# Kernel tuning notes

Measured on AMD Instinct MI355X. Metric: run time of the kernel, lower is better.

## Reference

```python
import jax, jax.numpy as jnp
import numpy as np

NUM_EXPERTS = 256
TOP_K = 8
HIDDEN = 7168
N_GROUP = 8
TOPK_GROUP = 4
ROUTED_SCALING_FACTOR = 2.5
NORM_TOPK_PROB = True
TOKENS = 8192


def setup_inputs() -> dict:
    key = jax.random.key(0)
    k1, k2, k3 = jax.random.split(key, 3)
    hidden_states = jax.random.normal(k1, (TOKENS, HIDDEN), dtype=jnp.float32)
    # small init scale keeps router logits in a reasonable sigmoid range
    weight = jax.random.normal(k2, (NUM_EXPERTS, HIDDEN), dtype=jnp.float32) * 0.02
    e_score_correction_bias = jax.random.normal(k3, (NUM_EXPERTS,), dtype=jnp.float32) * 0.01
    return {
        "hidden_states": hidden_states,
        "weight": weight,
        "e_score_correction_bias": e_score_correction_bias,
    }


def reference(hidden_states, weight, e_score_correction_bias):
    hs = hidden_states.reshape(-1, hidden_states.shape[-1]).astype(jnp.float32)
    # [T, E] router logits -> sigmoid scores
    router_logits = hs @ weight.astype(jnp.float32).T
    scores = jax.nn.sigmoid(router_logits)
    scores_for_choice = scores + e_score_correction_bias[None, :]

    experts_per_group = NUM_EXPERTS // N_GROUP
    T = scores_for_choice.shape[0]
    # group score = sum of top-2 biased scores within each group  [T, G]
    grouped = scores_for_choice.reshape(T, N_GROUP, experts_per_group)
    top2_vals, _ = jax.lax.top_k(grouped, 2)
    group_scores = top2_vals.sum(axis=-1)

    # select top groups and build group mask  [T, G]
    _, group_idx = jax.lax.top_k(group_scores, TOPK_GROUP)
    group_mask = jnp.zeros_like(group_scores).at[
        jnp.arange(T)[:, None], group_idx
    ].set(1.0)

    # expand group mask to experts and zero out non-selected groups  [T, E]
    score_mask = jnp.broadcast_to(
        group_mask[:, :, None], (T, N_GROUP, experts_per_group)
    ).reshape(T, NUM_EXPERTS)
    masked_scores = jnp.where(score_mask.astype(bool), scores_for_choice, 0.0)

    # top-k experts over masked biased scores, weights gathered from raw scores
    _, topk_indices = jax.lax.top_k(masked_scores, TOP_K)
    topk_weights = jnp.take_along_axis(scores, topk_indices, axis=1)
    if NORM_TOPK_PROB:
        topk_weights = topk_weights / (
            topk_weights.sum(axis=-1, keepdims=True) + 1e-20
        )
    topk_weights = topk_weights * ROUTED_SCALING_FACTOR
    return topk_indices, topk_weights
```

## Files before the change

### kernel.cpp

```cpp
#include <hip/hip_runtime.h>
#include <float.h>
#include <math.h>

#define TOKENS 8192
#define EXPERTS 256
#define HIDDEN 7168
#define TOPK 8
#define TOPKG 4

#define BM 128
#define BN 256
#define BK 32
#define KSPLIT 4
#define KQ (HIDDEN / KSPLIT)
#define NKTB (KQ / BK)

#define TAU_E 6.0e-6f
#define TAU_G 1.2e-5f
#define MAXFB 1024

#define WIMG_ELEMS 1835008

typedef __attribute__((ext_vector_type(8))) short bf16x8;
typedef __attribute__((ext_vector_type(16))) float f32x16;

__device__ inline ushort bf16_rne(float x) {
    uint u = __float_as_uint(x);
    return (ushort)((u + 0x7FFFu + ((u >> 16) & 1u)) >> 16);
}
__device__ inline float bf16_tof(ushort h) { return __uint_as_float((uint)h << 16); }

#define CVTPK(lo, hi) ({ uint r_; asm("v_cvt_pk_bf16_f32 %0, %1, %2" : "=v"(r_) : "v"(lo), "v"(hi)); r_; })
__device__ inline float lo16f(uint u) { return __uint_as_float(u << 16); }
__device__ inline float hi16f(uint u) { return __uint_as_float(u & 0xFFFF0000u); }

#define BAR() do {                                             \
    asm volatile("s_waitcnt lgkmcnt(0)" ::: "memory");         \
    __builtin_amdgcn_s_barrier();                              \
    __builtin_amdgcn_sched_barrier(0);                         \
} while (0)

__global__ __launch_bounds__(256) void split_w(const float* __restrict__ W,
                                               ushort* __restrict__ wh,
                                               ushort* __restrict__ wl,
                                               int* __restrict__ cnt) {
    if (blockIdx.x == 0 && threadIdx.x == 0) *cnt = 0;
    const int tau  = blockIdx.x * 256 + threadIdx.x;
    const int j    = tau & 7;
    const int lane = (tau >> 3) & 63;
    const int cg   = (tau >> 9) & 7;
    const int kt16 = tau >> 12;
    const int col  = cg * 32 + (lane & 31);
    const int k    = kt16 * 16 + (lane >> 5) * 8 + j;
    const float w  = W[(size_t)col * HIDDEN + k];
    const ushort h = bf16_rne(w);
    const ushort l = bf16_rne(w - bf16_tof(h));
    wh[tau] = h;
    wl[tau] = l;
}

template <bool ATOMIC>
__global__ __launch_bounds__(512, 2) void logits_mfma(const float* __restrict__ A,
                                                      const ushort* __restrict__ wh,
                                                      const ushort* __restrict__ wl,
                                                      float* __restrict__ dst) {
    __shared__ ushort Ah[2][BM * BK];
    __shared__ ushort Al[2][BM * BK];

    const int b  = blockIdx.x;
    const int ks = b & 3;
    const int mb = b >> 2;
    const int row0 = mb * BM;

    const int t = threadIdx.x, lane = t & 63, wid = t >> 6;
    const int wm = wid >> 2, wn = wid & 3;

    const int sr = t >> 2, q = t & 3;
    const float* Ap = A + (size_t)(row0 + sr) * HIDDEN + (size_t)ks * KQ + q * 8;
    const int sswz = ((sr >> 1) ^ (sr >> 3)) & 3;
    const int sidx = sr * 32 + ((q ^ sswz) << 3);

    int fidx[2][2];
    #pragma unroll
    for (int mi = 0; mi < 2; ++mi) {
        const int r = wm * 64 + mi * 32 + (lane & 31);
        const int swz = ((r >> 1) ^ (r >> 3)) & 3;
        #pragma unroll
        for (int kh = 0; kh < 2; ++kh)
            fidx[mi][kh] = r * 32 + (((kh * 2 + (lane >> 5)) ^ swz) << 3);
    }

    const int wlanes = lane * 8;

    f32x16 acc[2][2];
    #pragma unroll
    for (int mi = 0; mi < 2; ++mi)
        #pragma unroll
        for (int n = 0; n < 2; ++n) acc[mi][n] = (f32x16)0.f;

    float4 aA0, aA1, aB0, aB1;
    bf16x8 wAh[2][2], wAl[2][2], wBh[2][2], wBl[2][2];

    #define WLOAD(DH, DL, KTL) do {                                            \
        const size_t wo = ((size_t)((ks * NKTB + (KTL)) * 16 + wn * 2)) * 512 + wlanes; \
        DH[0][0] = *(const bf16x8*)(wh + wo);                                  \
        DH[1][0] = *(const bf16x8*)(wh + wo + 512);                            \
        DH[0][1] = *(const bf16x8*)(wh + wo + 4096);                           \
        DH[1][1] = *(const bf16x8*)(wh + wo + 4608);                           \
        DL[0][0] = *(const bf16x8*)(wl + wo);                                  \
        DL[1][0] = *(const bf16x8*)(wl + wo + 512);                            \
        DL[0][1] = *(const bf16x8*)(wl + wo + 4096);                           \
        DL[1][1] = *(const bf16x8*)(wl + wo + 4608);                           \
    } while (0)

    #define STAGE(BB, R0, R1) do {                                             \
        uint h0 = CVTPK(R0.x, R0.y), h1 = CVTPK(R0.z, R0.w);                   \
        uint h2 = CVTPK(R1.x, R1.y), h3 = CVTPK(R1.z, R1.w);                   \
        float q0 = R0.x - lo16f(h0), q1 = R0.y - hi16f(h0);                    \
        float q2 = R0.z - lo16f(h1), q3 = R0.w - hi16f(h1);                    \
        float q4 = R1.x - lo16f(h2), q5 = R1.y - hi16f(h2);                    \
        float q6 = R1.z - lo16f(h3), q7 = R1.w - hi16f(h3);                    \
        uint l0 = CVTPK(q0, q1), l1 = CVTPK(q2, q3);                           \
        uint l2 = CVTPK(q4, q5), l3 = CVTPK(q6, q7);                           \
        *(uint4*)&Ah[BB][sidx] = make_uint4(h0, h1, h2, h3);                   \
        *(uint4*)&Al[BB][sidx] = make_uint4(l0, l1, l2, l3);                   \
    } while (0)

    #define ALOAD(R0, R1, KTL) do {                                            \
        const int ka = ((KTL) < NKTB ? (KTL) : NKTB - 1) * BK;                 \
        R0 = *(const float4*)(Ap + ka);                                        \
        R1 = *(const float4*)(Ap + ka + 4);                                    \
    } while (0)

    #define MF __builtin_amdgcn_mfma_f32_32x32x16_bf16

    #define ITER(KT, BB, X0, X1, WXH, WXL, WYH, WYL) do {                      \
        BAR();                                                                 \
        bf16x8 afh[2][2], afl[2][2];                                           \
        afh[0][0] = *(const bf16x8*)&Ah[BB][fidx[0][0]];                       \
        afh[0][1] = *(const bf16x8*)&Ah[BB][fidx[0][1]];                       \
        afh[1][0] = *(const bf16x8*)&Ah[BB][fidx[1][0]];                       \
        afh[1][1] = *(const bf16x8*)&Ah[BB][fidx[1][1]];                       \
        afl[0][0] = *(const bf16x8*)&Al[BB][fidx[0][0]];                       \
        afl[0][1] = *(const bf16x8*)&Al[BB][fidx[0][1]];                       \
        afl[1][0] = *(const bf16x8*)&Al[BB][fidx[1][0]];                       \
        afl[1][1] = *(const bf16x8*)&Al[BB][fidx[1][1]];                       \
        STAGE((BB) ^ 1, X0, X1);                                               \
        ALOAD(X0, X1, (KT) + 3);                                               \
        WLOAD(WYH, WYL, ((KT) + 1 < NKTB ? (KT) + 1 : NKTB - 1));              \
        acc[0][0] = MF(afh[0][0], WXH[0][0], acc[0][0], 0, 0, 0);              \
        acc[0][0] = MF(afl[0][0], WXH[0][0], acc[0][0], 0, 0, 0);              \
        acc[0][0] = MF(afh[0][0], WXL[0][0], acc[0][0], 0, 0, 0);              \
        acc[0][1] = MF(afh[0][0], WXH[1][0], acc[0][1], 0, 0, 0);              \
        acc[0][1] = MF(afl[0][0], WXH[1][0], acc[0][1], 0, 0, 0);              \
        acc[0][1] = MF(afh[0][0], WXL[1][0], acc[0][1], 0, 0, 0);              \
        acc[1][0] = MF(afh[1][0], WXH[0][0], acc[1][0], 0, 0, 0);              \
        acc[1][0] = MF(afl[1][0], WXH[0][0], acc[1][0], 0, 0, 0);              \
        acc[1][0] = MF(afh[1][0], WXL[0][0], acc[1][0], 0, 0, 0);              \
        acc[1][1] = MF(afh[1][0], WXH[1][0], acc[1][1], 0, 0, 0);              \
        acc[1][1] = MF(afl[1][0], WXH[1][0], acc[1][1], 0, 0, 0);              \
        acc[1][1] = MF(afh[1][0], WXL[1][0], acc[1][1], 0, 0, 0);              \
        acc[0][0] = MF(afh[0][1], WXH[0][1], acc[0][0], 0, 0, 0);              \
        acc[0][0] = MF(afl[0][1], WXH[0][1], acc[0][0], 0, 0, 0);              \
        acc[0][0] = MF(afh[0][1], WXL[0][1], acc[0][0], 0, 0, 0);              \
        acc[0][1] = MF(afh[0][1], WXH[1][1], acc[0][1], 0, 0, 0);              \
        acc[0][1] = MF(afl[0][1], WXH[1][1], acc[0][1], 0, 0, 0);              \
        acc[0][1] = MF(afh[0][1], WXL[1][1], acc[0][1], 0, 0, 0);              \
        acc[1][0] = MF(afh[1][1], WXH[0][1], acc[1][0], 0, 0, 0);              \
        acc[1][0] = MF(afl[1][1], WXH[0][1], acc[1][0], 0, 0, 0);              \
        acc[1][0] = MF(afh[1][1], WXL[0][1], acc[1][0], 0, 0, 0);              \
        acc[1][1] = MF(afh[1][1], WXH[1][1], acc[1][1], 0, 0, 0);              \
        acc[1][1] = MF(afl[1][1], WXH[1][1], acc[1][1], 0, 0, 0);              \
        acc[1][1] = MF(afh[1][1], WXL[1][1], acc[1][1], 0, 0, 0);              \
    } while (0)

    ALOAD(aA0, aA1, 0);
    STAGE(0, aA0, aA1);
    ALOAD(aA0, aA1, 1);
    ALOAD(aB0, aB1, 2);
    WLOAD(wAh, wAl, 0);

    for (int kt2 = 0; kt2 < NKTB; kt2 += 2) {
        ITER(kt2,     0, aA0, aA1, wAh, wAl, wBh, wBl);
        ITER(kt2 + 1, 1, aB0, aB1, wBh, wBl, wAh, wAl);
    }

    float* o = ATOMIC ? dst : dst + (size_t)ks * TOKENS * EXPERTS;
    #pragma unroll
    for (int mi = 0; mi < 2; ++mi)
        #pragma unroll
        for (int n = 0; n < 2; ++n)
            #pragma unroll
            for (int g = 0; g < 16; ++g) {
                const int row = row0 + wm * 64 + mi * 32 + (g & 3) + ((g >> 2) << 3) + ((lane >> 5) << 2);
                const int col = wn * 64 + n * 32 + (lane & 31);
                const size_t idx = (size_t)row * EXPERTS + col;
                if (ATOMIC) atomicAdd(o + idx, acc[mi][n][g]);
                else        o[idx] = acc[mi][n][g];
            }
    #undef ITER
    #undef MF
    #undef ALOAD
    #undef STAGE
    #undef WLOAD
}

template <int NPART>
__global__ __launch_bounds__(256) void route_margin(const float* __restrict__ p0,
                                                    const float* __restrict__ bias,
                                                    float* __restrict__ out,
                                                    int* __restrict__ cnt,
                                                    int* __restrict__ list) {
    const int lane = threadIdx.x & 63;
    const int t    = blockIdx.x * 4 + (threadIdx.x >> 6);

    float4 lg = *(const float4*)(p0 + (size_t)t * EXPERTS + (lane << 2));
    #pragma unroll
    for (int p = 1; p < NPART; ++p) {
        const float4 l2 = *(const float4*)(p0 + (size_t)p * TOKENS * EXPERTS +
                                           (size_t)t * EXPERTS + (lane << 2));
        lg.x += l2.x; lg.y += l2.y; lg.z += l2.z; lg.w += l2.w;
    }
    const float4 bz = *(const float4*)(bias + (lane << 2));

    const float s0 = 1.f / (1.f + expf(-lg.x));
    const float s1 = 1.f / (1.f + expf(-lg.y));
    const float s2 = 1.f / (1.f + expf(-lg.z));
    const float s3 = 1.f / (1.f + expf(-lg.w));
    const float b0 = s0 + bz.x, b1 = s1 + bz.y, b2 = s2 + bz.z, b3 = s3 + bz.w;

    float hi01 = fmaxf(b0, b1), lo01 = fminf(b0, b1);
    float hi23 = fmaxf(b2, b3), lo23 = fminf(b2, b3);
    float a0v = fmaxf(hi01, hi23);
    float a1v = fmaxf(fminf(hi01, hi23), fmaxf(lo01, lo23));
    #pragma unroll
    for (int off = 1; off < 8; off <<= 1) {
        float o0 = __shfl_xor(a0v, off);
        float o1 = __shfl_xor(a1v, off);
        float n0 = fmaxf(a0v, o0);
        float n1 = fmaxf(fminf(a0v, o0), fmaxf(a1v, o1));
        a0v = n0; a1v = n1;
    }
    const float gscore = a0v + a1v;

    float gsc[8];
    #pragma unroll
    for (int g = 0; g < 8; ++g) gsc[g] = __shfl(gscore, g << 3);

    const int g0 = lane >> 3;
    int myrank = 0;
    float v4 = -1e30f, v5 = -1e30f;
    #pragma unroll
    for (int h = 0; h < 8; ++h) {
        int rk = 0;
        #pragma unroll
        for (int h2 = 0; h2 < 8; ++h2)
            rk += ((gsc[h2] > gsc[h]) || (gsc[h2] == gsc[h] && h2 < h)) ? 1 : 0;
        if (h == g0) myrank = rk;
        if (rk == TOPKG - 1) v4 = gsc[h];
        if (rk == TOPKG)     v5 = gsc[h];
    }
    const bool sel = (myrank < TOPKG);
    const float margin_g = v4 - v5;

    float m0 = sel ? b0 : 0.f;
    float m1 = sel ? b1 : 0.f;
    float m2 = sel ? b2 : 0.f;
    float m3 = sel ? b3 : 0.f;

    float sum = 0.f;
    int myidx = 0; float mysc = 0.f;
    float prev = 0.f, mine = 1e30f;
    #pragma unroll
    for (int rr = 0; rr < TOPK + 1; ++rr) {
        float bv = m0; int bj = 0;
        if (m1 > bv) { bv = m1; bj = 1; }
        if (m2 > bv) { bv = m2; bj = 2; }
        if (m3 > bv) { bv = m3; bj = 3; }
        float bsc = (bj == 0) ? s0 : (bj == 1) ? s1 : (bj == 2) ? s2 : s3;
        int bidx = (lane << 2) | bj;
        #pragma unroll
        for (int off = 1; off < 64; off <<= 1) {
            float ov  = __shfl_xor(bv, off);
            int   oi  = __shfl_xor(bidx, off);
            float osc = __shfl_xor(bsc, off);
            if (ov > bv || (ov == bv && oi < bidx)) { bv = ov; bidx = oi; bsc = osc; }
        }
        if (rr) mine = fminf(mine, prev - bv);
        prev = bv;
        if (rr < TOPK) {
            sum += bsc;
            if (lane == rr) { myidx = bidx; mysc = bsc; }
            if ((bidx >> 2) == lane) {
                const int sl = bidx & 3;
                if      (sl == 0) m0 = -FLT_MAX;
                else if (sl == 1) m1 = -FLT_MAX;
                else if (sl == 2) m2 = -FLT_MAX;
                else              m3 = -FLT_MAX;
            }
        }
    }

    const bool fb = (margin_g < TAU_G) || (mine < TAU_E);
    if (fb) {
        if (lane == 0) { int p = atomicAdd(cnt, 1); if (p < MAXFB) list[p] = t; }
    } else if (lane < TOPK) {
        const size_t base = (size_t)t * TOPK + lane;
        out[base] = (float)myidx;
        out[(size_t)TOKENS * TOPK + base] = mysc / (sum + 1e-20f) * 2.5f;
    }
}

__global__ __launch_bounds__(256) void fallback_logits(const float* __restrict__ A,
                                                       const float* __restrict__ W,
                                                       const int* __restrict__ cnt,
                                                       const int* __restrict__ list,
                                                       double* __restrict__ lgs) {
    const int n = min(*cnt, MAXFB);
    if (n == 0) return;
    __shared__ float Wsh[HIDDEN];
    const int e = blockIdx.x;
    const int tid = threadIdx.x;

    const float4* wg = (const float4*)(W + (size_t)e * HIDDEN);
    for (int i = tid; i < HIDDEN / 4; i += 256)
        ((float4*)Wsh)[i] = wg[i];
    __syncthreads();

    const int lane = tid & 63, wv = tid >> 6;
    for (int ti = wv; ti < n; ti += 4) {
        const int t = list[ti];
        const float* ar = A + (size_t)t * HIDDEN;
        double ac = 0.0;
        #pragma unroll 4
        for (int it = 0; it < HIDDEN / 256; ++it) {
            const int k = it * 256 + (lane << 2);
            const float4 a4 = *(const float4*)(ar + k);
            const float4 w4 = *(const float4*)&Wsh[k];
            ac = fma((double)a4.x, (double)w4.x, ac);
            ac = fma((double)a4.y, (double)w4.y, ac);
            ac = fma((double)a4.z, (double)w4.z, ac);
            ac = fma((double)a4.w, (double)w4.w, ac);
        }
        #pragma unroll
        for (int off = 32; off; off >>= 1)
            ac += __shfl_xor(ac, off);
        if (lane == 0)
            lgs[(size_t)ti * EXPERTS + e] = ac;
    }
}

__global__ __launch_bounds__(256) void fallback_route(const double* __restrict__ lgs,
                                                      const float* __restrict__ bias,
                                                      const int* __restrict__ cnt,
                                                      const int* __restrict__ list,
                                                      float* __restrict__ out) {
    const int n  = min(*cnt, MAXFB);
    const int ti = blockIdx.x * 4 + (threadIdx.x >> 6);
    if (ti >= n) return;
    const int lane = threadIdx.x & 63;
    const int t = list[ti];

    const double l0 = lgs[(size_t)ti * EXPERTS + (lane << 2)];
    const double l1 = lgs[(size_t)ti * EXPERTS + (lane << 2) + 1];
    const double l2 = lgs[(size_t)ti * EXPERTS + (lane << 2) + 2];
    const double l3 = lgs[(size_t)ti * EXPERTS + (lane << 2) + 3];
    const float4 bzf = *(const float4*)(bias + (lane << 2));

    const double s0 = 1.0 / (1.0 + exp(-l0));
    const double s1 = 1.0 / (1.0 + exp(-l1));
    const double s2 = 1.0 / (1.0 + exp(-l2));
    const double s3 = 1.0 / (1.0 + exp(-l3));
    const double b0 = s0 + (double)bzf.x, b1 = s1 + (double)bzf.y;
    const double b2 = s2 + (double)bzf.z, b3 = s3 + (double)bzf.w;

    double hi01 = fmax(b0, b1), lo01 = fmin(b0, b1);
    double hi23 = fmax(b2, b3), lo23 = fmin(b2, b3);
    double a0v = fmax(hi01, hi23);
    double a1v = fmax(fmin(hi01, hi23), fmax(lo01, lo23));
    #pragma unroll
    for (int off = 1; off < 8; off <<= 1) {
        double o0 = __shfl_xor(a0v, off);
        double o1 = __shfl_xor(a1v, off);
        double n0 = fmax(a0v, o0);
        double n1 = fmax(fmin(a0v, o0), fmax(a1v, o1));
        a0v = n0; a1v = n1;
    }
    const double gscore = a0v + a1v;
    double gsc[8];
    #pragma unroll
    for (int g = 0; g < 8; ++g) gsc[g] = __shfl(gscore, g << 3);
    const int g0 = lane >> 3;
    int rank = 0;
    #pragma unroll
    for (int h = 0; h < 8; ++h)
        rank += ((gsc[h] > gscore) || (gsc[h] == gscore && h < g0)) ? 1 : 0;
    const bool sel = (rank < TOPKG);

    double m0 = sel ? b0 : 0.0;
    double m1 = sel ? b1 : 0.0;
    double m2 = sel ? b2 : 0.0;
    double m3 = sel ? b3 : 0.0;

    double sum = 0.0;
    int myidx = 0; double mysc = 0.0;
    #pragma unroll
    for (int rr = 0; rr < TOPK; ++rr) {
        double bv = m0; int bj = 0;
        if (m1 > bv) { bv = m1; bj = 1; }
        if (m2 > bv) { bv = m2; bj = 2; }
        if (m3 > bv) { bv = m3; bj = 3; }
        double bsc = (bj == 0) ? s0 : (bj == 1) ? s1 : (bj == 2) ? s2 : s3;
        int bidx = (lane << 2) | bj;
        #pragma unroll
        for (int off = 1; off < 64; off <<= 1) {
            double ov  = __shfl_xor(bv, off);
            int    oi  = __shfl_xor(bidx, off);
            double osc = __shfl_xor(bsc, off);
            if (ov > bv || (ov == bv && oi < bidx)) { bv = ov; bidx = oi; bsc = osc; }
        }
        sum += bsc;
        if (lane == rr) { myidx = bidx; mysc = bsc; }
        if ((bidx >> 2) == lane) {
            const int sl = bidx & 3;
            if      (sl == 0) m0 = -DBL_MAX;
            else if (sl == 1) m1 = -DBL_MAX;
            else if (sl == 2) m2 = -DBL_MAX;
            else              m3 = -DBL_MAX;
        }
    }
    if (lane < TOPK) {
        const size_t base = (size_t)t * TOPK + lane;
        out[base] = (float)myidx;
        out[(size_t)TOKENS * TOPK + base] = (float)(mysc / (sum + 1e-20) * 2.5);
    }
}

extern "C" void kernel_launch(void* const* d_in, const int* in_sizes, int n_in,
                              void* d_out, int out_size, void* d_ws, size_t ws_size,
                              hipStream_t stream) {
    const float* hs   = (const float*)d_in[0];
    const float* wt   = (const float*)d_in[1];
    const float* bias = (const float*)d_in[2];
    float* out = (float*)d_out;
    char* ws = (char*)d_ws;

    const size_t LGSZ = (size_t)TOKENS * EXPERTS * 4;
    const size_t WIMG = (size_t)WIMG_ELEMS * 2;

    if (ws_size >= KSPLIT * LGSZ + 131072 + 2 * WIMG) {
        float*  part  = (float*)ws;
        int*    cnt   = (int*)(ws + KSPLIT * LGSZ);
        int*    list  = (int*)(ws + KSPLIT * LGSZ + 256);
        ushort* wsh   = (ushort*)(ws + KSPLIT * LGSZ + 131072);
        ushort* wsl   = (ushort*)(ws + KSPLIT * LGSZ + 131072 + WIMG);
        double* lgs64 = (double*)ws;

        split_w<<<WIMG_ELEMS / 256, 256, 0, stream>>>(wt, wsh, wsl, cnt);
        logits_mfma<false><<<256, 512, 0, stream>>>(hs, wsh, wsl, part);
        route_margin<KSPLIT><<<TOKENS / 4, 256, 0, stream>>>(part, bias, out, cnt, list);
        fallback_logits<<<EXPERTS, 256, 0, stream>>>(hs, wt, cnt, list, lgs64);
        fallback_route<<<MAXFB / 4, 256, 0, stream>>>(lgs64, bias, cnt, list, out);
    } else {
        float*  logits = (float*)ws;
        int*    cnt    = (int*)(ws + LGSZ);
        int*    list   = (int*)(ws + LGSZ + 256);
        ushort* wsh    = (ushort*)(ws + LGSZ + 131072);
        ushort* wsl    = (ushort*)(ws + LGSZ + 131072 + WIMG);
        double* lgs64  = (double*)ws;

        hipMemsetAsync(logits, 0, LGSZ, stream);
        split_w<<<WIMG_ELEMS / 256, 256, 0, stream>>>(wt, wsh, wsl, cnt);
        logits_mfma<true><<<256, 512, 0, stream>>>(hs, wsh, wsl, logits);
        route_margin<1><<<TOKENS / 4, 256, 0, stream>>>(logits, bias, out, cnt, list);
        fallback_logits<<<EXPERTS, 256, 0, stream>>>(hs, wt, cnt, list, lgs64);
        fallback_route<<<MAXFB / 4, 256, 0, stream>>>(lgs64, bias, cnt, list, out);
    }
}
```

Measured before the change: 211.9 us.

## Halve GEMM row tile to 64 and remap waves to one N-strip each

Cuts the logits GEMM row tile from 128 to 64 rows. Each of the 8 waves now covers a 32-column strip across all 64 rows instead of a 64x64 sub-tile, and the grid doubles from 256 to 512 blocks. The goal is to fill more of the GPU's compute units and cut per-thread register use (accumulators, weight fragments). The cost is that each weight fragment is reused across half as many rows, so weight traffic per output doubles and the A staging/swizzle indexing changes.

Measured after the change: 192.0 us. 1.1x faster.

```diff
diff --git a/kernel.cpp b/kernel.cpp
--- a/kernel.cpp
+++ b/kernel.cpp
@@ -8,7 +8,7 @@
 #define TOPK 8
 #define TOPKG 4
 
-#define BM 128
+#define BM 64
 #define BN 256
 #define BK 32
 #define KSPLIT 4
@@ -72,18 +72,17 @@
     const int mb = b >> 2;
     const int row0 = mb * BM;
 
-    const int t = threadIdx.x, lane = t & 63, wid = t >> 6;
-    const int wm = wid >> 2, wn = wid & 3;
-
-    const int sr = t >> 2, q = t & 3;
-    const float* Ap = A + (size_t)(row0 + sr) * HIDDEN + (size_t)ks * KQ + q * 8;
+    const int t = threadIdx.x, lane = t & 63, wn = t >> 6;
+
+    const int sr = t >> 3, q = t & 7;
+    const float* Ap = A + (size_t)(row0 + sr) * HIDDEN + (size_t)ks * KQ + q * 4;
     const int sswz = ((sr >> 1) ^ (sr >> 3)) & 3;
-    const int sidx = sr * 32 + ((q ^ sswz) << 3);
+    const int sidx = sr * 32 + ((((q >> 1)) ^ sswz) << 3) + (q & 1) * 4;
 
     int fidx[2][2];
     #pragma unroll
     for (int mi = 0; mi < 2; ++mi) {
-        const int r = wm * 64 + mi * 32 + (lane & 31);
+        const int r = mi * 32 + (lane & 31);
         const int swz = ((r >> 1) ^ (r >> 3)) & 3;
         #pragma unroll
         for (int kh = 0; kh < 2; ++kh)
@@ -92,49 +91,38 @@
 
     const int wlanes = lane * 8;
 
-    f32x16 acc[2][2];
-    #pragma unroll
-    for (int mi = 0; mi < 2; ++mi)
-        #pragma unroll
-        for (int n = 0; n < 2; ++n) acc[mi][n] = (f32x16)0.f;
-
-    float4 aA0, aA1, aB0, aB1;
-    bf16x8 wAh[2][2], wAl[2][2], wBh[2][2], wBl[2][2];
+    f32x16 acc[2];
+    acc[0] = (f32x16)0.f;
+    acc[1] = (f32x16)0.f;
+
+    float4 aA, aB;
+    bf16x8 wAh[2], wAl[2], wBh[2], wBl[2];
 
     #define WLOAD(DH, DL, KTL) do {                                            \
-        const size_t wo = ((size_t)((ks * NKTB + (KTL)) * 16 + wn * 2)) * 512 + wlanes; \
-        DH[0][0] = *(const bf16x8*)(wh + wo);                                  \
-        DH[1][0] = *(const bf16x8*)(wh + wo + 512);                            \
-        DH[0][1] = *(const bf16x8*)(wh + wo + 4096);                           \
-        DH[1][1] = *(const bf16x8*)(wh + wo + 4608);                           \
-        DL[0][0] = *(const bf16x8*)(wl + wo);                                  \
-        DL[1][0] = *(const bf16x8*)(wl + wo + 512);                            \
-        DL[0][1] = *(const bf16x8*)(wl + wo + 4096);                           \
-        DL[1][1] = *(const bf16x8*)(wl + wo + 4608);                           \
+        const size_t wo = ((size_t)((ks * NKTB + (KTL)) * 2) * 8 + wn) * 512 + wlanes; \
+        DH[0] = *(const bf16x8*)(wh + wo);                                     \
+        DH[1] = *(const bf16x8*)(wh + wo + 4096);                              \
+        DL[0] = *(const bf16x8*)(wl + wo);                                     \
+        DL[1] = *(const bf16x8*)(wl + wo + 4096);                              \
     } while (0)
 
-    #define STAGE(BB, R0, R1) do {                                             \
-        uint h0 = CVTPK(R0.x, R0.y), h1 = CVTPK(R0.z, R0.w);                   \
-        uint h2 = CVTPK(R1.x, R1.y), h3 = CVTPK(R1.z, R1.w);                   \
-        float q0 = R0.x - lo16f(h0), q1 = R0.y - hi16f(h0);                    \
-        float q2 = R0.z - lo16f(h1), q3 = R0.w - hi16f(h1);                    \
-        float q4 = R1.x - lo16f(h2), q5 = R1.y - hi16f(h2);                    \
-        float q6 = R1.z - lo16f(h3), q7 = R1.w - hi16f(h3);                    \
+    #define STAGE(BB, R) do {                                                  \
+        uint h0 = CVTPK(R.x, R.y), h1 = CVTPK(R.z, R.w);                       \
+        float q0 = R.x - lo16f(h0), q1 = R.y - hi16f(h0);                      \
+        float q2 = R.z - lo16f(h1), q3 = R.w - hi16f(h1);                      \
         uint l0 = CVTPK(q0, q1), l1 = CVTPK(q2, q3);                           \
-        uint l2 = CVTPK(q4, q5), l3 = CVTPK(q6, q7);                           \
-        *(uint4*)&Ah[BB][sidx] = make_uint4(h0, h1, h2, h3);                   \
-        *(uint4*)&Al[BB][sidx] = make_uint4(l0, l1, l2, l3);                   \
+        *(uint2*)&Ah[BB][sidx] = make_uint2(h0, h1);                           \
+        *(uint2*)&Al[BB][sidx] = make_uint2(l0, l1);                           \
     } while (0)
 
-    #define ALOAD(R0, R1, KTL) do {                                            \
+    #define ALOAD(R, KTL) do {                                                 \
         const int ka = ((KTL) < NKTB ? (KTL) : NKTB - 1) * BK;                 \
-        R0 = *(const float4*)(Ap + ka);                                        \
-        R1 = *(const float4*)(Ap + ka + 4);                                    \
+        R = *(const float4*)(Ap + ka);                                         \
     } while (0)
 
     #define MF __builtin_amdgcn_mfma_f32_32x32x16_bf16
 
-    #define ITER(KT, BB, X0, X1, WXH, WXL, WYH, WYL) do {                      \
+    #define ITER(KT, BB, X, WXH, WXL, WYH, WYL) do {                           \
         BAR();                                                                 \
         bf16x8 afh[2][2], afl[2][2];                                           \
         afh[0][0] = *(const bf16x8*)&Ah[BB][fidx[0][0]];                       \
@@ -145,59 +133,45 @@
         afl[0][1] = *(const bf16x8*)&Al[BB][fidx[0][1]];                       \
         afl[1][0] = *(const bf16x8*)&Al[BB][fidx[1][0]];                       \
         afl[1][1] = *(const bf16x8*)&Al[BB][fidx[1][1]];                       \
-        STAGE((BB) ^ 1, X0, X1);                                               \
-        ALOAD(X0, X1, (KT) + 3);                                               \
+        STAGE((BB) ^ 1, X);                                                    \
+        ALOAD(X, (KT) + 3);                                                    \
         WLOAD(WYH, WYL, ((KT) + 1 < NKTB ? (KT) + 1 : NKTB - 1));              \
-        acc[0][0] = MF(afh[0][0], WXH[0][0], acc[0][0], 0, 0, 0);              \
-        acc[0][0] = MF(afl[0][0], WXH[0][0], acc[0][0], 0, 0, 0);              \
-        acc[0][0] = MF(afh[0][0], WXL[0][0], acc[0][0], 0, 0, 0);              \
-        acc[0][1] = MF(afh[0][0], WXH[1][0], acc[0][1], 0, 0, 0);              \
-        acc[0][1] = MF(afl[0][0], WXH[1][0], acc[0][1], 0, 0, 0);              \
-        acc[0][1] = MF(afh[0][0], WXL[1][0], acc[0][1], 0, 0, 0);              \
-        acc[1][0] = MF(afh[1][0], WXH[0][0], acc[1][0], 0, 0, 0);              \
-        acc[1][0] = MF(afl[1][0], WXH[0][0], acc[1][0], 0, 0, 0);              \
-        acc[1][0] = MF(afh[1][0], WXL[0][0], acc[1][0], 0, 0, 0);              \
-        acc[1][1] = MF(afh[1][0], WXH[1][0], acc[1][1], 0, 0, 0);              \
-        acc[1][1] = MF(afl[1][0], WXH[1][0], acc[1][1], 0, 0, 0);              \
-        acc[1][1] = MF(afh[1][0], WXL[1][0], acc[1][1], 0, 0, 0);              \
-        acc[0][0] = MF(afh[0][1], WXH[0][1], acc[0][0], 0, 0, 0);              \
-        acc[0][0] = MF(afl[0][1], WXH[0][1], acc[0][0], 0, 0, 0);              \
-        acc[0][0] = MF(afh[0][1], WXL[0][1], acc[0][0], 0, 0, 0);              \
-        acc[0][1] = MF(afh[0][1], WXH[1][1], acc[0][1], 0, 0, 0);              \
-        acc[0][1] = MF(afl[0][1], WXH[1][1], acc[0][1], 0, 0, 0);              \
-        acc[0][1] = MF(afh[0][1], WXL[1][1], acc[0][1], 0, 0, 0);              \
-        acc[1][0] = MF(afh[1][1], WXH[0][1], acc[1][0], 0, 0, 0);              \
-        acc[1][0] = MF(afl[1][1], WXH[0][1], acc[1][0], 0, 0, 0);              \
-        acc[1][0] = MF(afh[1][1], WXL[0][1], acc[1][0], 0, 0, 0);              \
-        acc[1][1] = MF(afh[1][1], WXH[1][1], acc[1][1], 0, 0, 0);              \
-        acc[1][1] = MF(afl[1][1], WXH[1][1], acc[1][1], 0, 0, 0);              \
-        acc[1][1] = MF(afh[1][1], WXL[1][1], acc[1][1], 0, 0, 0);              \
+        acc[0] = MF(afh[0][0], WXH[0], acc[0], 0, 0, 0);                       \
+        acc[0] = MF(afl[0][0], WXH[0], acc[0], 0, 0, 0);                       \
+        acc[0] = MF(afh[0][0], WXL[0], acc[0], 0, 0, 0);                       \
+        acc[1] = MF(afh[1][0], WXH[0], acc[1], 0, 0, 0);                       \
+        acc[1] = MF(afl[1][0], WXH[0], acc[1], 0, 0, 0);                       \
+        acc[1] = MF(afh[1][0], WXL[0], acc[1], 0, 0, 0);                       \
+        acc[0] = MF(afh[0][1], WXH[1], acc[0], 0, 0, 0);                       \
+        acc[0] = MF(afl[0][1], WXH[1], acc[0], 0, 0, 0);                       \
+        acc[0] = MF(afh[0][1], WXL[1], acc[0], 0, 0, 0);                       \
+        acc[1] = MF(afh[1][1], WXH[1], acc[1], 0, 0, 0);                       \
+        acc[1] = MF(afl[1][1], WXH[1], acc[1], 0, 0, 0);                       \
+        acc[1] = MF(afh[1][1], WXL[1], acc[1], 0, 0, 0);                       \
     } while (0)
 
-    ALOAD(aA0, aA1, 0);
-    STAGE(0, aA0, aA1);
-    ALOAD(aA0, aA1, 1);
-    ALOAD(aB0, aB1, 2);
+    ALOAD(aA, 0);
+    STAGE(0, aA);
+    ALOAD(aA, 1);
+    ALOAD(aB, 2);
     WLOAD(wAh, wAl, 0);
 
     for (int kt2 = 0; kt2 < NKTB; kt2 += 2) {
-        ITER(kt2,     0, aA0, aA1, wAh, wAl, wBh, wBl);
-        ITER(kt2 + 1, 1, aB0, aB1, wBh, wBl, wAh, wAl);
+        ITER(kt2,     0, aA, wAh, wAl, wBh, wBl);
+        ITER(kt2 + 1, 1, aB, wBh, wBl, wAh, wAl);
     }
 
     float* o = ATOMIC ? dst : dst + (size_t)ks * TOKENS * EXPERTS;
     #pragma unroll
     for (int mi = 0; mi < 2; ++mi)
         #pragma unroll
-        for (int n = 0; n < 2; ++n)
-            #pragma unroll
-            for (int g = 0; g < 16; ++g) {
-                const int row = row0 + wm * 64 + mi * 32 + (g & 3) + ((g >> 2) << 3) + ((lane >> 5) << 2);
-                const int col = wn * 64 + n * 32 + (lane & 31);
-                const size_t idx = (size_t)row * EXPERTS + col;
-                if (ATOMIC) atomicAdd(o + idx, acc[mi][n][g]);
-                else        o[idx] = acc[mi][n][g];
-            }
+        for (int g = 0; g < 16; ++g) {
+            const int row = row0 + mi * 32 + (g & 3) + ((g >> 2) << 3) + ((lane >> 5) << 2);
+            const int col = wn * 32 + (lane & 31);
+            const size_t idx = (size_t)row * EXPERTS + col;
+            if (ATOMIC) atomicAdd(o + idx, acc[mi][g]);
+            else        o[idx] = acc[mi][g];
+        }
     #undef ITER
     #undef MF
     #undef ALOAD
@@ -447,6 +421,7 @@
 
     const size_t LGSZ = (size_t)TOKENS * EXPERTS * 4;
     const size_t WIMG = (size_t)WIMG_ELEMS * 2;
+    const int NBLK = (TOKENS / BM) * KSPLIT;
 
     if (ws_size >= KSPLIT * LGSZ + 131072 + 2 * WIMG) {
         float*  part  = (float*)ws;
@@ -457,7 +432,7 @@
         double* lgs64 = (double*)ws;
 
         split_w<<<WIMG_ELEMS / 256, 256, 0, stream>>>(wt, wsh, wsl, cnt);
-        logits_mfma<false><<<256, 512, 0, stream>>>(hs, wsh, wsl, part);
+        logits_mfma<false><<<NBLK, 512, 0, stream>>>(hs, wsh, wsl, part);
         route_margin<KSPLIT><<<TOKENS / 4, 256, 0, stream>>>(part, bias, out, cnt, list);
         fallback_logits<<<EXPERTS, 256, 0, stream>>>(hs, wt, cnt, list, lgs64);
         fallback_route<<<MAXFB / 4, 256, 0, stream>>>(lgs64, bias, cnt, list, out);
@@ -471,7 +446,7 @@
 
         hipMemsetAsync(logits, 0, LGSZ, stream);
         split_w<<<WIMG_ELEMS / 256, 256, 0, stream>>>(wt, wsh, wsl, cnt);
-        logits_mfma<true><<<256, 512, 0, stream>>>(hs, wsh, wsl, logits);
+        logits_mfma<true><<<NBLK, 512, 0, stream>>>(hs, wsh, wsl, logits);
         route_margin<1><<<TOKENS / 4, 256, 0, stream>>>(logits, bias, out, cnt, list);
         fallback_logits<<<EXPERTS, 256, 0, stream>>>(hs, wt, cnt, list, lgs64);
         fallback_route<<<MAXFB / 4, 256, 0, stream>>>(lgs64, bias, cnt, list, out);
```
